# Kernel optimization log

Measured on AMD Instinct MI355X. Metric: run time of the kernel, lower is better.

The kernel has to match this reference:

```python
import jax, jax.numpy as jnp
import numpy as np

B, T = 64, 256
IN, HID, OUT = 512, 1024, 256
NUM_DOMAINS = 20

def setup_inputs() -> dict:
    key = jax.random.key(0)
    k1, k2, k3, k4 = jax.random.split(key, 4)
    x = jax.random.normal(k1, (B, T, IN), dtype=jnp.float32)
    hetero_info = jax.random.randint(k2, (B, 2), 0, NUM_DOMAINS, dtype=jnp.int64)
    # embedding tables init N(0, 0.02) as in the torch module
    fc1_table = 0.02 * jax.random.normal(k3, (NUM_DOMAINS, IN * HID + HID), dtype=jnp.float32)
    fc2_table = 0.02 * jax.random.normal(k4, (NUM_DOMAINS, HID * OUT + OUT), dtype=jnp.float32)
    return {"x": x, "hetero_info": hetero_info, "fc1_table": fc1_table, "fc2_table": fc2_table}

def reference(x, hetero_info, fc1_table, fc2_table):
    domain_id = hetero_info[:, 0].astype(jnp.int32)
    Bn = domain_id.shape[0]
    fc1_param = fc1_table[domain_id]                     # (B, IN*HID + HID)
    w1 = fc1_param[:, : IN * HID].reshape(Bn, IN, HID)   # (B, IN, HID)
    b1 = fc1_param[:, IN * HID:].reshape(Bn, 1, HID)
    fc2_param = fc2_table[domain_id]                     # (B, HID*OUT + OUT)
    w2 = fc2_param[:, : HID * OUT].reshape(Bn, HID, OUT) # (B, HID, OUT)
    b2 = fc2_param[:, HID * OUT:].reshape(Bn, 1, OUT)
    h = jnp.einsum('bti,bih->bth', x, w1) + b1
    h = jax.nn.gelu(h, approximate=False)  # torch nn.GELU default = exact erf
    out = jnp.einsum('bth,bho->bto', h, w2) + b2
    return out
```

## Files before the change

kernel.cpp:

```cpp
#include <hip/hip_runtime.h>
#include <math.h>

#define B_  64
#define T_  256
#define IN_ 512
#define HID_ 1024
#define OUT_ 256
#define NDOM 20

typedef __bf16 bf16_t;
typedef __bf16 bf16x8 __attribute__((ext_vector_type(8)));
typedef float  f32x4  __attribute__((ext_vector_type(4)));

__device__ __forceinline__ unsigned f2bf_bits(float f) {
    unsigned u = __builtin_bit_cast(unsigned, f);
    return (u + 0x7FFFu + ((u >> 16) & 1u)) >> 16;
}
__device__ __forceinline__ unsigned pack_bf16x2(float x, float y) {
    return f2bf_bits(x) | (f2bf_bits(y) << 16);
}

__device__ __forceinline__ void gl_lds16(const void* g, void* l) {
    __builtin_amdgcn_global_load_lds(
        (const __attribute__((address_space(1))) unsigned*)g,
        (__attribute__((address_space(3))) unsigned*)l,
        16, 0, 0);
}

__global__ __launch_bounds__(256) void cvt_x(
    const float* __restrict__ X, bf16_t* __restrict__ Xbf)
{
    const size_t idx = (size_t)blockIdx.x * 256 + threadIdx.x;
    float4 v = ((const float4*)X)[idx];
    uint2 p;
    p.x = pack_bf16x2(v.x, v.y);
    p.y = pack_bf16x2(v.z, v.w);
    ((uint2*)Xbf)[idx] = p;
}

template<int K, int N>
__global__ __launch_bounds__(256) void cvt_transpose(
    const float* __restrict__ table, bf16_t* __restrict__ Wt, float* __restrict__ BiasOut)
{
    const int d  = blockIdx.z;
    const float* W = table + (size_t)d * ((size_t)K * N + N);
    const int n0 = blockIdx.x * 64;
    const int k0 = blockIdx.y * 64;
    const int tid = threadIdx.x;

    __shared__ float t[64][65];

    #pragma unroll
    for (int r = 0; r < 4; ++r) {
        const int kl = (tid >> 4) + r * 16;
        const int nl = (tid & 15) * 4;
        float4 v = *(const float4*)(W + (size_t)(k0 + kl) * N + n0 + nl);
        t[kl][nl + 0] = v.x; t[kl][nl + 1] = v.y;
        t[kl][nl + 2] = v.z; t[kl][nl + 3] = v.w;
    }
    __syncthreads();

    bf16_t* Wtd = Wt + (size_t)d * K * N;
    #pragma unroll
    for (int r = 0; r < 4; ++r) {
        const int nl = (tid >> 4) + r * 16;
        const int k4 = (tid & 15) * 4;
        uint2 p;
        p.x = pack_bf16x2(t[k4 + 0][nl], t[k4 + 1][nl]);
        p.y = pack_bf16x2(t[k4 + 2][nl], t[k4 + 3][nl]);
        *(uint2*)(Wtd + (size_t)(n0 + nl) * K + k0 + k4) = p;
    }

    if (blockIdx.y == 0 && tid < 64)
        BiasOut[(size_t)d * N + n0 + tid] = W[(size_t)K * N + n0 + tid];
}

#define CT_STRIDE 136
__global__ __launch_bounds__(256) void fc1_gemm(
    const bf16_t* __restrict__ Xbf,
    const bf16_t* __restrict__ W1t,
    const float*  __restrict__ Bias,
    const int*    __restrict__ hetero,
    bf16_t*       __restrict__ H)
{
    const int id   = blockIdx.x;
    const int g    = id & 127;
    const int nidx = id >> 7;
    const int b    = g >> 1;
    const int m0   = (g & 1) * 128;
    const int n0   = nidx * 128;
    const int d    = hetero[2 * b];
    const bf16_t* W    = W1t + (size_t)d * HID_ * IN_;
    const float*  bias = Bias + (size_t)d * HID_;
    const bf16_t* A    = Xbf + (size_t)(b * 256 + m0) * IN_;

    __shared__ __attribute__((aligned(16))) char smem[128 * CT_STRIDE * 2];
    bf16_t* LdsA = (bf16_t*)smem;
    bf16_t* LdsB = (bf16_t*)(smem + 16384);
    bf16_t* Ct   = (bf16_t*)smem;

    const int tid  = threadIdx.x;
    const int wave = tid >> 6;
    const int lane = tid & 63;
    const int l16  = lane & 15;
    const int quad = lane >> 4;
    const int wm   = (wave >> 1) * 64;
    const int wn   = (wave & 1) * 64;

    f32x4 acc[4][4] = {};

    for (int kk = 0; kk < IN_; kk += 64) {
        #pragma unroll
        for (int cc = 0; cc < 4; ++cc) {
            const int r0  = wave * 32 + cc * 8;
            const int row = r0 + (lane >> 3);
            const int cs  = (lane & 7) ^ (row & 7);
            gl_lds16(A + (size_t)row * IN_ + kk + cs * 8, &LdsA[r0 * 64]);
        }
        #pragma unroll
        for (int cc = 0; cc < 4; ++cc) {
            const int r0  = wave * 32 + cc * 8;
            const int row = r0 + (lane >> 3);
            const int cs  = (lane & 7) ^ (row & 7);
            gl_lds16(W + (size_t)(n0 + row) * IN_ + kk + cs * 8, &LdsB[r0 * 64]);
        }
        __syncthreads();

        #pragma unroll
        for (int h = 0; h < 2; ++h) {
            bf16x8 af[4], bfg[4];
            #pragma unroll
            for (int i = 0; i < 4; ++i) {
                const int r = wm + i * 16 + l16;
                const int c = (h * 4 + quad) ^ (r & 7);
                af[i] = *(const bf16x8*)&LdsA[r * 64 + c * 8];
            }
            #pragma unroll
            for (int j = 0; j < 4; ++j) {
                const int r = wn + j * 16 + l16;
                const int c = (h * 4 + quad) ^ (r & 7);
                bfg[j] = *(const bf16x8*)&LdsB[r * 64 + c * 8];
            }
            #pragma unroll
            for (int i = 0; i < 4; ++i)
                #pragma unroll
                for (int j = 0; j < 4; ++j)
                    acc[i][j] = __builtin_amdgcn_mfma_f32_16x16x32_bf16(bfg[j], af[i], acc[i][j], 0, 0, 0);
        }
        __syncthreads();
    }

    #pragma unroll
    for (int i = 0; i < 4; ++i) {
        const int m = wm + i * 16 + l16;
        #pragma unroll
        for (int j = 0; j < 4; ++j) {
            const int nl = wn + j * 16 + quad * 4;
            const float4 b4 = *(const float4*)&bias[n0 + nl];
            float v0 = acc[i][j][0] + b4.x;
            float v1 = acc[i][j][1] + b4.y;
            float v2 = acc[i][j][2] + b4.z;
            float v3 = acc[i][j][3] + b4.w;
            v0 = 0.5f * v0 * (1.0f + erff(v0 * 0.70710678f));
            v1 = 0.5f * v1 * (1.0f + erff(v1 * 0.70710678f));
            v2 = 0.5f * v2 * (1.0f + erff(v2 * 0.70710678f));
            v3 = 0.5f * v3 * (1.0f + erff(v3 * 0.70710678f));
            uint2 p;
            p.x = pack_bf16x2(v0, v1);
            p.y = pack_bf16x2(v2, v3);
            *(uint2*)&Ct[m * CT_STRIDE + nl] = p;
        }
    }
    __syncthreads();

    #pragma unroll
    for (int it = 0; it < 8; ++it) {
        const int row = it * 16 + (tid >> 4);
        const int ch  = tid & 15;
        uint4 v = *(const uint4*)&Ct[row * CT_STRIDE + ch * 8];
        *(uint4*)&H[((size_t)(b * 256 + m0 + row)) * HID_ + n0 + ch * 8] = v;
    }
}

__global__ __launch_bounds__(256) void fc2_gemm(
    const bf16_t* __restrict__ H,
    const bf16_t* __restrict__ W2t,
    const float*  __restrict__ Bias,
    const int*    __restrict__ hetero,
    float*        __restrict__ Out)
{
    const int id   = blockIdx.x;
    const int g    = id & 255;
    const int nidx = id >> 8;
    const int b    = g >> 2;
    const int m0   = (g & 3) * 64;
    const int n0   = nidx * 64;
    const int d    = hetero[2 * b];
    const bf16_t* W    = W2t + (size_t)d * OUT_ * HID_;
    const float*  bias = Bias + (size_t)d * OUT_;

    __shared__ __attribute__((aligned(16))) bf16_t LdsA[64 * 64];
    __shared__ __attribute__((aligned(16))) bf16_t LdsB[64 * 64];

    const int tid  = threadIdx.x;
    const int wave = tid >> 6;
    const int lane = tid & 63;
    const int l16  = lane & 15;
    const int quad = lane >> 4;
    const int wm   = (wave >> 1) * 32;
    const int wn   = (wave & 1) * 32;

    f32x4 acc[2][2] = {};

    for (int kk = 0; kk < HID_; kk += 64) {
        #pragma unroll
        for (int cc = 0; cc < 2; ++cc) {
            const int r0  = wave * 16 + cc * 8;
            const int row = r0 + (lane >> 3);
            const int cs  = (lane & 7) ^ (row & 7);
            gl_lds16(H + (size_t)(b * 256 + m0 + row) * HID_ + kk + cs * 8,
                     &LdsA[r0 * 64]);
        }
        #pragma unroll
        for (int cc = 0; cc < 2; ++cc) {
            const int r0  = wave * 16 + cc * 8;
            const int row = r0 + (lane >> 3);
            const int cs  = (lane & 7) ^ (row & 7);
            gl_lds16(W + (size_t)(n0 + row) * HID_ + kk + cs * 8,
                     &LdsB[r0 * 64]);
        }
        __syncthreads();

        #pragma unroll
        for (int h = 0; h < 2; ++h) {
            bf16x8 af[2], bfg[2];
            #pragma unroll
            for (int i = 0; i < 2; ++i) {
                const int r = wm + i * 16 + l16;
                const int c = (h * 4 + quad) ^ (r & 7);
                af[i] = *(const bf16x8*)&LdsA[r * 64 + c * 8];
            }
            #pragma unroll
            for (int j = 0; j < 2; ++j) {
                const int r = wn + j * 16 + l16;
                const int c = (h * 4 + quad) ^ (r & 7);
                bfg[j] = *(const bf16x8*)&LdsB[r * 64 + c * 8];
            }
            #pragma unroll
            for (int i = 0; i < 2; ++i)
                #pragma unroll
                for (int j = 0; j < 2; ++j)
                    acc[i][j] = __builtin_amdgcn_mfma_f32_16x16x32_bf16(bfg[j], af[i], acc[i][j], 0, 0, 0);
        }
        __syncthreads();
    }

    #pragma unroll
    for (int i = 0; i < 2; ++i) {
        const int m = m0 + wm + i * 16 + l16;
        #pragma unroll
        for (int j = 0; j < 2; ++j) {
            const int nl = wn + j * 16 + quad * 4;
            const float4 b4 = *(const float4*)&bias[n0 + nl];
            float4 o;
            o.x = acc[i][j][0] + b4.x;
            o.y = acc[i][j][1] + b4.y;
            o.z = acc[i][j][2] + b4.z;
            o.w = acc[i][j][3] + b4.w;
            *(float4*)&Out[(size_t)(b * 256 + m) * OUT_ + n0 + nl] = o;
        }
    }
}

extern "C" void kernel_launch(void* const* d_in, const int* in_sizes, int n_in,
                              void* d_out, int out_size, void* d_ws, size_t ws_size,
                              hipStream_t stream) {
    const float* x         = (const float*)d_in[0];
    const int*   hetero    = (const int*)d_in[1];
    const float* fc1_table = (const float*)d_in[2];
    const float* fc2_table = (const float*)d_in[3];
    float*       out       = (float*)d_out;

    char* ws = (char*)d_ws;
    bf16_t* W1t = (bf16_t*)(ws);
    bf16_t* W2t = (bf16_t*)(ws + 20971520);
    float*  b1  = (float*)(ws + 31457280);
    float*  b2  = (float*)(ws + 31539200);
    bf16_t* H   = (bf16_t*)(ws + 31559680);

    bf16_t* Xbf = (bf16_t*)d_out;

    cvt_x<<<dim3(8192), 256, 0, stream>>>(x, Xbf);
    cvt_transpose<IN_, HID_><<<dim3(HID_ / 64, IN_ / 64, NDOM), 256, 0, stream>>>(
        fc1_table, W1t, b1);
    cvt_transpose<HID_, OUT_><<<dim3(OUT_ / 64, HID_ / 64, NDOM), 256, 0, stream>>>(
        fc2_table, W2t, b2);

    fc1_gemm<<<dim3(1024), 256, 0, stream>>>(Xbf, W1t, b1, hetero, H);
    fc2_gemm<<<dim3(1024), 256, 0, stream>>>(H, W2t, b2, hetero, out);
}
```

Before: 188.5 us.

## Fuse x conversion into fc1, double-buffer both GEMMs, use fast GELU

Removes the separate fp32-to-bf16 pass over x. fc1 now loads fp32 x into registers, converts it and writes it to LDS itself. Both GEMM kernels get double-buffered LDS so loads for the next K step overlap compute on the current one. The libm erff in GELU is replaced by the Abramowitz-Stegun polynomial using a hardware reciprocal and exp, trading a little accuracy for fewer instructions. The doubled LDS footprint (64KB in fc1) may reduce occupancy.

Result: no change. 186.5 us (-1.1%).

```diff
diff --git a/kernel.cpp b/kernel.cpp
--- a/kernel.cpp
+++ b/kernel.cpp
@@ -10,6 +10,7 @@
 
 typedef __bf16 bf16_t;
 typedef __bf16 bf16x8 __attribute__((ext_vector_type(8)));
+typedef __bf16 bf16x4 __attribute__((ext_vector_type(4)));
 typedef float  f32x4  __attribute__((ext_vector_type(4)));
 
 __device__ __forceinline__ unsigned f2bf_bits(float f) {
@@ -27,15 +28,19 @@
         16, 0, 0);
 }
 
-__global__ __launch_bounds__(256) void cvt_x(
-    const float* __restrict__ X, bf16_t* __restrict__ Xbf)
-{
-    const size_t idx = (size_t)blockIdx.x * 256 + threadIdx.x;
-    float4 v = ((const float4*)X)[idx];
-    uint2 p;
-    p.x = pack_bf16x2(v.x, v.y);
-    p.y = pack_bf16x2(v.z, v.w);
-    ((uint2*)Xbf)[idx] = p;
+__device__ __forceinline__ float gelu_fast(float v) {
+    const float t = v * 0.70710678118654752f;
+    const float a = __builtin_fabsf(t);
+    const float k = __builtin_amdgcn_rcpf(__builtin_fmaf(0.3275911f, a, 1.0f));
+    float p = __builtin_fmaf(1.061405429f, k, -1.453152027f);
+    p = __builtin_fmaf(p, k, 1.421413741f);
+    p = __builtin_fmaf(p, k, -0.284496736f);
+    p = __builtin_fmaf(p, k, 0.254829592f);
+    p = p * k;
+    const float e  = __expf(-a * a);
+    const float er = __builtin_fmaf(-p, e, 1.0f);
+    const float erf_t = __builtin_copysignf(er, t);
+    return 0.5f * v * (1.0f + erf_t);
 }
 
 template<int K, int N>
@@ -77,7 +82,7 @@
 
 #define CT_STRIDE 136
 __global__ __launch_bounds__(256) void fc1_gemm(
-    const bf16_t* __restrict__ Xbf,
+    const float*  __restrict__ X,
     const bf16_t* __restrict__ W1t,
     const float*  __restrict__ Bias,
     const int*    __restrict__ hetero,
@@ -92,12 +97,9 @@
     const int d    = hetero[2 * b];
     const bf16_t* W    = W1t + (size_t)d * HID_ * IN_;
     const float*  bias = Bias + (size_t)d * HID_;
-    const bf16_t* A    = Xbf + (size_t)(b * 256 + m0) * IN_;
-
-    __shared__ __attribute__((aligned(16))) char smem[128 * CT_STRIDE * 2];
-    bf16_t* LdsA = (bf16_t*)smem;
-    bf16_t* LdsB = (bf16_t*)(smem + 16384);
-    bf16_t* Ct   = (bf16_t*)smem;
+    const float*  A    = X + (size_t)(b * 256 + m0) * IN_;
+
+    __shared__ __attribute__((aligned(16))) char smem[65536];
 
     const int tid  = threadIdx.x;
     const int wave = tid >> 6;
@@ -107,25 +109,41 @@
     const int wm   = (wave >> 1) * 64;
     const int wn   = (wave & 1) * 64;
 
+    const int arow0 = tid >> 4;
+    const int acol4 = tid & 15;
+
     f32x4 acc[4][4] = {};
-
-    for (int kk = 0; kk < IN_; kk += 64) {
+    float4 pre[8];
+
+    auto ldsA = [&](int nb) -> bf16_t* { return (bf16_t*)(smem + nb * 16384); };
+    auto ldsB = [&](int nb) -> bf16_t* { return (bf16_t*)(smem + 32768 + nb * 16384); };
+
+    auto loadA = [&](int kk) {
+        #pragma unroll
+        for (int r = 0; r < 8; ++r)
+            pre[r] = *(const float4*)(A + (size_t)(arow0 + r * 16) * IN_ + kk + acol4 * 4);
+    };
+    auto writeA = [&](bf16_t* dst) {
+        #pragma unroll
+        for (int r = 0; r < 8; ++r) {
+            const int row = arow0 + r * 16;
+            const int cs  = (acol4 >> 1) ^ (row & 7);
+            bf16x4 w;
+            w[0] = (bf16_t)pre[r].x; w[1] = (bf16_t)pre[r].y;
+            w[2] = (bf16_t)pre[r].z; w[3] = (bf16_t)pre[r].w;
+            *(bf16x4*)&dst[row * 64 + cs * 8 + (acol4 & 1) * 4] = w;
+        }
+    };
+    auto stageB = [&](int kk, bf16_t* dst) {
         #pragma unroll
         for (int cc = 0; cc < 4; ++cc) {
             const int r0  = wave * 32 + cc * 8;
             const int row = r0 + (lane >> 3);
             const int cs  = (lane & 7) ^ (row & 7);
-            gl_lds16(A + (size_t)row * IN_ + kk + cs * 8, &LdsA[r0 * 64]);
-        }
-        #pragma unroll
-        for (int cc = 0; cc < 4; ++cc) {
-            const int r0  = wave * 32 + cc * 8;
-            const int row = r0 + (lane >> 3);
-            const int cs  = (lane & 7) ^ (row & 7);
-            gl_lds16(W + (size_t)(n0 + row) * IN_ + kk + cs * 8, &LdsB[r0 * 64]);
-        }
-        __syncthreads();
-
+            gl_lds16(W + (size_t)(n0 + row) * IN_ + kk + cs * 8, dst + r0 * 64);
+        }
+    };
+    auto compute = [&](const bf16_t* La, const bf16_t* Lb) {
         #pragma unroll
         for (int h = 0; h < 2; ++h) {
             bf16x8 af[4], bfg[4];
@@ -133,13 +151,13 @@
             for (int i = 0; i < 4; ++i) {
                 const int r = wm + i * 16 + l16;
                 const int c = (h * 4 + quad) ^ (r & 7);
-                af[i] = *(const bf16x8*)&LdsA[r * 64 + c * 8];
+                af[i] = *(const bf16x8*)&La[r * 64 + c * 8];
             }
             #pragma unroll
             for (int j = 0; j < 4; ++j) {
                 const int r = wn + j * 16 + l16;
                 const int c = (h * 4 + quad) ^ (r & 7);
-                bfg[j] = *(const bf16x8*)&LdsB[r * 64 + c * 8];
+                bfg[j] = *(const bf16x8*)&Lb[r * 64 + c * 8];
             }
             #pragma unroll
             for (int i = 0; i < 4; ++i)
@@ -147,8 +165,26 @@
                 for (int j = 0; j < 4; ++j)
                     acc[i][j] = __builtin_amdgcn_mfma_f32_16x16x32_bf16(bfg[j], af[i], acc[i][j], 0, 0, 0);
         }
+    };
+
+    loadA(0);
+    stageB(0, ldsB(0));
+    writeA(ldsA(0));
+    __syncthreads();
+
+    int buf = 0;
+    for (int s = 0; s < 7; ++s) {
+        loadA((s + 1) * 64);
+        stageB((s + 1) * 64, ldsB(buf ^ 1));
+        compute(ldsA(buf), ldsB(buf));
+        writeA(ldsA(buf ^ 1));
         __syncthreads();
-    }
+        buf ^= 1;
+    }
+    compute(ldsA(buf), ldsB(buf));
+    __syncthreads();
+
+    bf16_t* Ct = (bf16_t*)smem;
 
     #pragma unroll
     for (int i = 0; i < 4; ++i) {
@@ -157,18 +193,12 @@
         for (int j = 0; j < 4; ++j) {
             const int nl = wn + j * 16 + quad * 4;
             const float4 b4 = *(const float4*)&bias[n0 + nl];
-            float v0 = acc[i][j][0] + b4.x;
-            float v1 = acc[i][j][1] + b4.y;
-            float v2 = acc[i][j][2] + b4.z;
-            float v3 = acc[i][j][3] + b4.w;
-            v0 = 0.5f * v0 * (1.0f + erff(v0 * 0.70710678f));
-            v1 = 0.5f * v1 * (1.0f + erff(v1 * 0.70710678f));
-            v2 = 0.5f * v2 * (1.0f + erff(v2 * 0.70710678f));
-            v3 = 0.5f * v3 * (1.0f + erff(v3 * 0.70710678f));
-            uint2 p;
-            p.x = pack_bf16x2(v0, v1);
-            p.y = pack_bf16x2(v2, v3);
-            *(uint2*)&Ct[m * CT_STRIDE + nl] = p;
+            bf16x4 w;
+            w[0] = (bf16_t)gelu_fast(acc[i][j][0] + b4.x);
+            w[1] = (bf16_t)gelu_fast(acc[i][j][1] + b4.y);
+            w[2] = (bf16_t)gelu_fast(acc[i][j][2] + b4.z);
+            w[3] = (bf16_t)gelu_fast(acc[i][j][3] + b4.w);
+            *(bf16x4*)&Ct[m * CT_STRIDE + nl] = w;
         }
     }
     __syncthreads();
@@ -199,8 +229,8 @@
     const bf16_t* W    = W2t + (size_t)d * OUT_ * HID_;
     const float*  bias = Bias + (size_t)d * OUT_;
 
-    __shared__ __attribute__((aligned(16))) bf16_t LdsA[64 * 64];
-    __shared__ __attribute__((aligned(16))) bf16_t LdsB[64 * 64];
+    __shared__ __attribute__((aligned(16))) bf16_t LdsA[2][64 * 64];
+    __shared__ __attribute__((aligned(16))) bf16_t LdsB[2][64 * 64];
 
     const int tid  = threadIdx.x;
     const int wave = tid >> 6;
@@ -212,25 +242,19 @@
 
     f32x4 acc[2][2] = {};
 
-    for (int kk = 0; kk < HID_; kk += 64) {
+    auto stage = [&](int kk, int nb) {
         #pragma unroll
         for (int cc = 0; cc < 2; ++cc) {
             const int r0  = wave * 16 + cc * 8;
             const int row = r0 + (lane >> 3);
             const int cs  = (lane & 7) ^ (row & 7);
             gl_lds16(H + (size_t)(b * 256 + m0 + row) * HID_ + kk + cs * 8,
-                     &LdsA[r0 * 64]);
-        }
-        #pragma unroll
-        for (int cc = 0; cc < 2; ++cc) {
-            const int r0  = wave * 16 + cc * 8;
-            const int row = r0 + (lane >> 3);
-            const int cs  = (lane & 7) ^ (row & 7);
+                     &LdsA[nb][r0 * 64]);
             gl_lds16(W + (size_t)(n0 + row) * HID_ + kk + cs * 8,
-                     &LdsB[r0 * 64]);
-        }
-        __syncthreads();
-
+                     &LdsB[nb][r0 * 64]);
+        }
+    };
+    auto compute = [&](int nb) {
         #pragma unroll
         for (int h = 0; h < 2; ++h) {
             bf16x8 af[2], bfg[2];
@@ -238,13 +262,13 @@
             for (int i = 0; i < 2; ++i) {
                 const int r = wm + i * 16 + l16;
                 const int c = (h * 4 + quad) ^ (r & 7);
-                af[i] = *(const bf16x8*)&LdsA[r * 64 + c * 8];
+                af[i] = *(const bf16x8*)&LdsA[nb][r * 64 + c * 8];
             }
             #pragma unroll
             for (int j = 0; j < 2; ++j) {
                 const int r = wn + j * 16 + l16;
                 const int c = (h * 4 + quad) ^ (r & 7);
-                bfg[j] = *(const bf16x8*)&LdsB[r * 64 + c * 8];
+                bfg[j] = *(const bf16x8*)&LdsB[nb][r * 64 + c * 8];
             }
             #pragma unroll
             for (int i = 0; i < 2; ++i)
@@ -252,8 +276,18 @@
                 for (int j = 0; j < 2; ++j)
                     acc[i][j] = __builtin_amdgcn_mfma_f32_16x16x32_bf16(bfg[j], af[i], acc[i][j], 0, 0, 0);
         }
+    };
+
+    stage(0, 0);
+    __syncthreads();
+    int buf = 0;
+    for (int s = 0; s < 15; ++s) {
+        stage((s + 1) * 64, buf ^ 1);
+        compute(buf);
         __syncthreads();
-    }
+        buf ^= 1;
+    }
+    compute(buf);
 
     #pragma unroll
     for (int i = 0; i < 2; ++i) {
@@ -288,14 +322,11 @@
     float*  b2  = (float*)(ws + 31539200);
     bf16_t* H   = (bf16_t*)(ws + 31559680);
 
-    bf16_t* Xbf = (bf16_t*)d_out;
-
-    cvt_x<<<dim3(8192), 256, 0, stream>>>(x, Xbf);
     cvt_transpose<IN_, HID_><<<dim3(HID_ / 64, IN_ / 64, NDOM), 256, 0, stream>>>(
         fc1_table, W1t, b1);
     cvt_transpose<HID_, OUT_><<<dim3(OUT_ / 64, HID_ / 64, NDOM), 256, 0, stream>>>(
         fc2_table, W2t, b2);
 
-    fc1_gemm<<<dim3(1024), 256, 0, stream>>>(Xbf, W1t, b1, hetero, H);
+    fc1_gemm<<<dim3(1024), 256, 0, stream>>>(x, W1t, b1, hetero, H);
     fc2_gemm<<<dim3(1024), 256, 0, stream>>>(H, W2t, b2, hetero, out);
 }
```
